# Kernel optimization log

Measured on AMD Instinct MI355X. Metric: run time of the kernel, lower is better.

Reference implementation:

```python
import jax, jax.numpy as jnp
import numpy as np

B, F, DOF, N_CLS = 256, 1024, 64, 1000

def setup_inputs() -> dict:
    key = jax.random.key(0)
    k1, k2 = jax.random.split(key)
    x = jax.random.normal(k1, (B, F), dtype=jnp.float32)
    # min/max of the input domain, as the dataloader scan would estimate on randn data
    min_x = jnp.array([-3.0], dtype=jnp.float32)
    max_x = jnp.array([3.0], dtype=jnp.float32)
    W = jax.random.normal(k2, (N_CLS, F * DOF), dtype=jnp.float32) * 0.01
    return {"x": x, "min_x": min_x, "max_x": max_x, "W": W, "dof": DOF}


def _lagrange_embed(x, min_x, max_x, dof):
    # 1D P1 Lagrange basis. simplices[t] = (t+1, t), t = 0..dof-2.
    b_, f_ = x.shape
    T = dof - 1
    h = 1.0 / T  # uniform mesh spacing on [0, 1]
    # normalize to unit interval, flatten to scalar stream of length b = B*F
    xn = ((x.reshape(-1, 1) - min_x) / (max_x - min_x)).reshape(-1)  # (b,)
    t = jnp.arange(T, dtype=xn.dtype)                                 # (T,)
    s = xn[:, None] / h                                               # (b, T) broadcastable
    lam0 = s - t            # barycentric coord of vertex t+1  (b, T)
    lam1 = (t + 1.0) - s    # barycentric coord of vertex t    (b, T)
    n2t = ((lam0 >= 0.0) & (lam1 >= 0.0)).astype(xn.dtype)            # (b, T)
    z = jnp.zeros((xn.shape[0], 1), dtype=xn.dtype)
    # mask[b, p] = number of active simplices touching vertex p (scatter of n2t to p=t and p=t+1)
    mask = jnp.concatenate([n2t, z], axis=1) + jnp.concatenate([z, n2t], axis=1)  # (b, dof)
    # shape_values[b, p] = sum over active simplices of the barycentric value at vertex p
    w0 = n2t * lam0  # goes to vertex p = t+1
    w1 = n2t * lam1  # goes to vertex p = t
    shape_vals = jnp.concatenate([w1, z], axis=1) + jnp.concatenate([z, w0], axis=1)  # (b, dof)
    basis = shape_vals / jnp.maximum(mask, 1.0)
    # rescale back to the input domain (n_features == 1, so (1,) broadcasts)
    emb = basis * (max_x - min_x) + min_x  # (b, dof)
    return emb.reshape(b_, f_ * dof)


def reference(x, min_x, max_x, W, dof):
    emb = jax.lax.stop_gradient(_lagrange_embed(x, min_x, max_x, dof))  # .detach() in torch
    return emb @ W.T  # bias-free Linear: (B, n_cls)
```

## Files before the change

### kernel.cpp

```cpp
#include <hip/hip_runtime.h>
#include <hip/hip_bf16.h>
#include <cstdint>

#define NB 256
#define NF 1024
#define NDOF 64
#define NCLS 1000
#define CTILE 128
#define FGROUP 32
#define NFB (NF / FGROUP)
#define ROWSTR 68

typedef __attribute__((ext_vector_type(8))) short short8;
typedef __attribute__((ext_vector_type(16))) float floatx16;

static __device__ inline unsigned short bfu(float f) {
    __hip_bfloat16 h = __float2bfloat16(f);
    union { __hip_bfloat16 h; unsigned short u; } cv;
    cv.h = h;
    return cv.u;
}

__global__ __launch_bounds__(256) void lagr_meta(
    const float* __restrict__ x, const float* __restrict__ mnp,
    const float* __restrict__ mxp, uint2* __restrict__ meta)
{
    __shared__ uint2 tile[32][33];
    int f0 = blockIdx.x * 32;
    int b0 = blockIdx.y * 32;
    int tid = threadIdx.x;
    float mn = mnp[0], mx = mxp[0];
    float scale = mx - mn;
    float inv = 63.0f / scale;

    int fl = tid & 31, br = tid >> 5;
#pragma unroll
    for (int i = 0; i < 4; ++i) {
        int bl = br + i * 8;
        float xv = x[(size_t)(b0 + bl) * NF + f0 + fl];
        float s = (xv - mn) * inv;
        float wA = 0.0f, wB = 0.0f;
        uint32_t t = 0u;
        if (s >= 0.0f && s <= 63.0f) {
            float tf = floorf(s);
            if (tf > 62.0f) tf = 62.0f;
            t  = (uint32_t)tf;
            wA = scale * (tf + 1.0f - s);
            wB = scale * (s - tf);
        }
        uint32_t P0 = (uint32_t)bfu(wA) | ((uint32_t)bfu(wB) << 16);
        tile[fl][bl] = make_uint2(P0, t);
    }
    __syncthreads();
    int bl = tid & 31, fr = tid >> 5;
#pragma unroll
    for (int i = 0; i < 4; ++i) {
        int f = fr + i * 8;
        meta[(size_t)(f0 + f) * NB + b0 + bl] = tile[f][bl];
    }
}

__global__ __launch_bounds__(512, 2) void lagr_main(
    const uint2* __restrict__ meta, const float* __restrict__ W,
    const float* __restrict__ mnp, float* __restrict__ part)
{
    __shared__ unsigned short wt[2][CTILE * ROWSTR];
    __shared__ float bias_s[CTILE];

    int tid  = threadIdx.x;
    int lane = tid & 63;
    int wave = tid >> 6;
    int half8 = (lane >> 5) << 3;
    int c0 = blockIdx.y * CTILE;
    int f0 = blockIdx.x * FGROUP;

    int cst = tid >> 2;
    int q4  = tid & 3;
    int crow = c0 + cst;
    if (crow > NCLS - 1) crow = NCLS - 1;
    const float* wrow = W + (size_t)crow * (NF * NDOF);

    floatx16 acc0, acc1, acc2, acc3;
#pragma unroll
    for (int r = 0; r < 16; ++r) { acc0[r] = 0.0f; acc1[r] = 0.0f; acc2[r] = 0.0f; acc3[r] = 0.0f; }
    float rowsum = 0.0f;

    float4 st[4];
    auto issue = [&](int f) {
        const float4* src = (const float4*)(wrow + ((size_t)f << 6)) + (q4 << 2);
        st[0] = src[0];
        st[1] = src[1];
        st[2] = src[2];
        st[3] = src[3];
    };
    auto commit = [&](unsigned short* buf) {
        float v[16] = { st[0].x, st[0].y, st[0].z, st[0].w,
                        st[1].x, st[1].y, st[1].z, st[1].w,
                        st[2].x, st[2].y, st[2].z, st[2].w,
                        st[3].x, st[3].y, st[3].z, st[3].w };
        uint32_t d[8];
#pragma unroll
        for (int i = 0; i < 8; ++i) {
            rowsum += v[2 * i] + v[2 * i + 1];
            d[i] = (uint32_t)bfu(v[2 * i]) | ((uint32_t)bfu(v[2 * i + 1]) << 16);
        }
        unsigned short* dst = buf + cst * ROWSTR + (q4 << 4);
        ((uint2*)dst)[0] = make_uint2(d[0], d[1]);
        ((uint2*)dst)[1] = make_uint2(d[2], d[3]);
        ((uint2*)dst)[2] = make_uint2(d[4], d[5]);
        ((uint2*)dst)[3] = make_uint2(d[6], d[7]);
    };

    unsigned short* cur = &wt[0][0];
    unsigned short* nxt = &wt[1][0];

    const uint2* mbase = meta + wave * 32 + (lane & 31);
    uint2 mcur = mbase[(size_t)f0 * NB];

    issue(f0);
    commit(cur);
    __syncthreads();

#pragma unroll 1
    for (int ch = 0; ch < FGROUP; ++ch) {
        int f = f0 + ch;
        bool more = (ch + 1 < FGROUP);
        if (more) issue(f + 1);
        uint2 mnext = mcur;
        if (more) mnext = mbase[(size_t)(f + 1) * NB];

        uint32_t P0 = mcur.x;
        uint32_t t  = mcur.y;
        uint32_t odd = t & 1u;
        uint32_t X0 = odd ? (P0 << 16) : P0;
        uint32_t X1 = odd ? (P0 >> 16) : 0u;
        int d0 = (int)(t & ~1u) - half8;

        short8 afrag[4];
#pragma unroll
        for (int kc = 0; kc < 4; ++kc) {
            union { uint32_t u[4]; short8 v; } a;
#pragma unroll
            for (int q = 0; q < 4; ++q) {
                int C = kc * 16 + 2 * q;
                a.u[q] = (d0 == C) ? X0 : (d0 == C - 2) ? X1 : 0u;
            }
            afrag[kc] = a.v;
        }

        const unsigned short* rb = cur + (lane & 31) * ROWSTR + half8;
#define CTBODY(CT, ACC) { \
        const unsigned short* r = rb + (CT) * 32 * ROWSTR; \
        _Pragma("unroll") \
        for (int kc = 0; kc < 4; ++kc) { \
            union { uint2 u2[2]; short8 v; } bf; \
            bf.u2[0] = *(const uint2*)(r + kc * 16); \
            bf.u2[1] = *(const uint2*)(r + kc * 16 + 4); \
            ACC = __builtin_amdgcn_mfma_f32_32x32x16_bf16(afrag[kc], bf.v, ACC, 0, 0, 0); \
        } }
        CTBODY(0, acc0)
        CTBODY(1, acc1)
        CTBODY(2, acc2)
        CTBODY(3, acc3)
#undef CTBODY

        if (more) commit(nxt);
        unsigned short* tmp = cur; cur = nxt; nxt = tmp;
        mcur = mnext;
        __syncthreads();
    }

    rowsum += __shfl_xor(rowsum, 1);
    rowsum += __shfl_xor(rowsum, 2);
    if (q4 == 0) bias_s[cst] = mnp[0] * rowsum;
    __syncthreads();

    float* pslice = part + (size_t)blockIdx.x * NB * NCLS;
    int col = lane & 31;
    int rowhi = (lane >> 5) << 2;
#define EPI(CT, ACC) { \
        int c = c0 + (CT) * 32 + col; \
        if (c < NCLS) { \
            float bias = bias_s[(CT) * 32 + col]; \
            _Pragma("unroll") \
            for (int r = 0; r < 16; ++r) { \
                int brow = (r & 3) + 8 * (r >> 2) + rowhi; \
                pslice[(size_t)(wave * 32 + brow) * NCLS + c] = ACC[r] + bias; \
            } } }
    EPI(0, acc0)
    EPI(1, acc1)
    EPI(2, acc2)
    EPI(3, acc3)
#undef EPI
}

__global__ __launch_bounds__(256) void lagr_reduce(
    const float* __restrict__ part, float* __restrict__ out)
{
    int i = blockIdx.x * blockDim.x + threadIdx.x;
    const float4* p = (const float4*)part;
    float4 a0 = make_float4(0.f, 0.f, 0.f, 0.f), a1 = a0, a2 = a0, a3 = a0;
    const int S = NB * NCLS / 4;
#pragma unroll
    for (int fb = 0; fb < NFB; fb += 4) {
        float4 v0 = p[(size_t)(fb + 0) * S + i];
        float4 v1 = p[(size_t)(fb + 1) * S + i];
        float4 v2 = p[(size_t)(fb + 2) * S + i];
        float4 v3 = p[(size_t)(fb + 3) * S + i];
        a0.x += v0.x; a0.y += v0.y; a0.z += v0.z; a0.w += v0.w;
        a1.x += v1.x; a1.y += v1.y; a1.z += v1.z; a1.w += v1.w;
        a2.x += v2.x; a2.y += v2.y; a2.z += v2.z; a2.w += v2.w;
        a3.x += v3.x; a3.y += v3.y; a3.z += v3.z; a3.w += v3.w;
    }
    float4 r;
    r.x = (a0.x + a1.x) + (a2.x + a3.x);
    r.y = (a0.y + a1.y) + (a2.y + a3.y);
    r.z = (a0.z + a1.z) + (a2.z + a3.z);
    r.w = (a0.w + a1.w) + (a2.w + a3.w);
    ((float4*)out)[i] = r;
}

extern "C" void kernel_launch(void* const* d_in, const int* in_sizes, int n_in,
                              void* d_out, int out_size, void* d_ws, size_t ws_size,
                              hipStream_t stream) {
    const float* x  = (const float*)d_in[0];
    const float* mn = (const float*)d_in[1];
    const float* mx = (const float*)d_in[2];
    const float* W  = (const float*)d_in[3];
    float* out = (float*)d_out;
    uint2* meta = (uint2*)d_ws;
    float* part = (float*)((char*)d_ws + (size_t)NF * NB * 8);

    lagr_meta<<<dim3(NF / 32, NB / 32), dim3(256), 0, stream>>>(x, mn, mx, meta);

    dim3 grid(NF / FGROUP, (NCLS + CTILE - 1) / CTILE);
    lagr_main<<<grid, dim3(512), 0, stream>>>(meta, W, mn, part);

    lagr_reduce<<<dim3(NB * NCLS / 4 / 256), dim3(256), 0, stream>>>(part, out);
}
```

Before: 385.2 us.

## Fuse embedding metadata computation into main GEMM kernel and XOR-swizzle weight LDS tile

Removes the separate meta kernel: each main block now computes the per-(b,f) bf16 weight pair and simplex index for its 32 features directly from x and stores them in shared memory. This drops one launch and the global round-trip of the meta buffer. The cost is that each of the 8 class-tile blocks per feature group repeats the x reads and arithmetic. The W tile in LDS also switches from a padded stride-68 layout to an XOR-swizzled 64-wide layout, so B fragments load as 16-byte reads and bank conflicts are avoided. Shared memory use grows, which may affect the two-blocks-per-CU occupancy.

```diff
diff --git a/kernel.cpp b/kernel.cpp
--- a/kernel.cpp
+++ b/kernel.cpp
@@ -9,7 +9,6 @@
 #define CTILE 128
 #define FGROUP 32
 #define NFB (NF / FGROUP)
-#define ROWSTR 68
 
 typedef __attribute__((ext_vector_type(8))) short short8;
 typedef __attribute__((ext_vector_type(16))) float floatx16;
@@ -21,61 +20,32 @@
     return cv.u;
 }
 
-__global__ __launch_bounds__(256) void lagr_meta(
+__global__ __launch_bounds__(512, 2) void lagr_main(
     const float* __restrict__ x, const float* __restrict__ mnp,
-    const float* __restrict__ mxp, uint2* __restrict__ meta)
+    const float* __restrict__ mxp, const float* __restrict__ W,
+    float* __restrict__ part)
 {
-    __shared__ uint2 tile[32][33];
-    int f0 = blockIdx.x * 32;
-    int b0 = blockIdx.y * 32;
-    int tid = threadIdx.x;
+    __shared__ unsigned short wt[2][128 * 64];
+    __shared__ uint32_t mP0[FGROUP][NB + 1];
+    __shared__ uint8_t  mT [FGROUP][NB + 8];
+    __shared__ float bias_s[CTILE];
+
+    int tid  = threadIdx.x;
+    int lane = tid & 63;
+    int wave = tid >> 6;
+    int hf   = lane >> 5;
+    int half8 = hf << 3;
+    int l7   = lane & 7;
+    int c0 = blockIdx.y * CTILE;
+    int f0 = blockIdx.x * FGROUP;
+
     float mn = mnp[0], mx = mxp[0];
     float scale = mx - mn;
     float inv = 63.0f / scale;
 
-    int fl = tid & 31, br = tid >> 5;
-#pragma unroll
-    for (int i = 0; i < 4; ++i) {
-        int bl = br + i * 8;
-        float xv = x[(size_t)(b0 + bl) * NF + f0 + fl];
-        float s = (xv - mn) * inv;
-        float wA = 0.0f, wB = 0.0f;
-        uint32_t t = 0u;
-        if (s >= 0.0f && s <= 63.0f) {
-            float tf = floorf(s);
-            if (tf > 62.0f) tf = 62.0f;
-            t  = (uint32_t)tf;
-            wA = scale * (tf + 1.0f - s);
-            wB = scale * (s - tf);
-        }
-        uint32_t P0 = (uint32_t)bfu(wA) | ((uint32_t)bfu(wB) << 16);
-        tile[fl][bl] = make_uint2(P0, t);
-    }
-    __syncthreads();
-    int bl = tid & 31, fr = tid >> 5;
-#pragma unroll
-    for (int i = 0; i < 4; ++i) {
-        int f = fr + i * 8;
-        meta[(size_t)(f0 + f) * NB + b0 + bl] = tile[f][bl];
-    }
-}
-
-__global__ __launch_bounds__(512, 2) void lagr_main(
-    const uint2* __restrict__ meta, const float* __restrict__ W,
-    const float* __restrict__ mnp, float* __restrict__ part)
-{
-    __shared__ unsigned short wt[2][CTILE * ROWSTR];
-    __shared__ float bias_s[CTILE];
-
-    int tid  = threadIdx.x;
-    int lane = tid & 63;
-    int wave = tid >> 6;
-    int half8 = (lane >> 5) << 3;
-    int c0 = blockIdx.y * CTILE;
-    int f0 = blockIdx.x * FGROUP;
-
     int cst = tid >> 2;
     int q4  = tid & 3;
+    int r7w = cst & 7;
     int crow = c0 + cst;
     if (crow > NCLS - 1) crow = NCLS - 1;
     const float* wrow = W + (size_t)crow * (NF * NDOF);
@@ -104,33 +74,50 @@
             rowsum += v[2 * i] + v[2 * i + 1];
             d[i] = (uint32_t)bfu(v[2 * i]) | ((uint32_t)bfu(v[2 * i + 1]) << 16);
         }
-        unsigned short* dst = buf + cst * ROWSTR + (q4 << 4);
-        ((uint2*)dst)[0] = make_uint2(d[0], d[1]);
-        ((uint2*)dst)[1] = make_uint2(d[2], d[3]);
-        ((uint2*)dst)[2] = make_uint2(d[4], d[5]);
-        ((uint2*)dst)[3] = make_uint2(d[6], d[7]);
+        unsigned short* row = buf + cst * 64;
+        *(uint4*)(row + (((2 * q4)     ^ r7w) << 3)) = make_uint4(d[0], d[1], d[2], d[3]);
+        *(uint4*)(row + (((2 * q4 + 1) ^ r7w) << 3)) = make_uint4(d[4], d[5], d[6], d[7]);
     };
 
     unsigned short* cur = &wt[0][0];
     unsigned short* nxt = &wt[1][0];
 
-    const uint2* mbase = meta + wave * 32 + (lane & 31);
-    uint2 mcur = mbase[(size_t)f0 * NB];
-
     issue(f0);
+
+    {
+        int fl = tid & 31, bq = tid >> 5;
+#pragma unroll
+        for (int i = 0; i < 16; ++i) {
+            int b = bq + i * 16;
+            float xv = x[(size_t)b * NF + f0 + fl];
+            float s = (xv - mn) * inv;
+            float wA = 0.0f, wB = 0.0f;
+            uint32_t t = 0u;
+            if (s >= 0.0f && s <= 63.0f) {
+                float tf = floorf(s);
+                if (tf > 62.0f) tf = 62.0f;
+                t  = (uint32_t)tf;
+                wA = scale * (tf + 1.0f - s);
+                wB = scale * (s - tf);
+            }
+            mP0[fl][b] = (uint32_t)bfu(wA) | ((uint32_t)bfu(wB) << 16);
+            mT[fl][b]  = (uint8_t)t;
+        }
+    }
+
     commit(cur);
     __syncthreads();
+
+    int mb = wave * 32 + (lane & 31);
 
 #pragma unroll 1
     for (int ch = 0; ch < FGROUP; ++ch) {
         int f = f0 + ch;
         bool more = (ch + 1 < FGROUP);
         if (more) issue(f + 1);
-        uint2 mnext = mcur;
-        if (more) mnext = mbase[(size_t)(f + 1) * NB];
-
-        uint32_t P0 = mcur.x;
-        uint32_t t  = mcur.y;
+
+        uint32_t P0 = mP0[ch][mb];
+        uint32_t t  = mT[ch][mb];
         uint32_t odd = t & 1u;
         uint32_t X0 = odd ? (P0 << 16) : P0;
         uint32_t X1 = odd ? (P0 >> 16) : 0u;
@@ -148,15 +135,12 @@
             afrag[kc] = a.v;
         }
 
-        const unsigned short* rb = cur + (lane & 31) * ROWSTR + half8;
 #define CTBODY(CT, ACC) { \
-        const unsigned short* r = rb + (CT) * 32 * ROWSTR; \
+        const unsigned short* rrow = cur + (size_t)((lane & 31) + 32 * (CT)) * 64; \
         _Pragma("unroll") \
         for (int kc = 0; kc < 4; ++kc) { \
-            union { uint2 u2[2]; short8 v; } bf; \
-            bf.u2[0] = *(const uint2*)(r + kc * 16); \
-            bf.u2[1] = *(const uint2*)(r + kc * 16 + 4); \
-            ACC = __builtin_amdgcn_mfma_f32_32x32x16_bf16(afrag[kc], bf.v, ACC, 0, 0, 0); \
+            short8 bv = *(const short8*)(rrow + (((2 * kc + hf) ^ l7) << 3)); \
+            ACC = __builtin_amdgcn_mfma_f32_32x32x16_bf16(afrag[kc], bv, ACC, 0, 0, 0); \
         } }
         CTBODY(0, acc0)
         CTBODY(1, acc1)
@@ -166,18 +150,17 @@
 
         if (more) commit(nxt);
         unsigned short* tmp = cur; cur = nxt; nxt = tmp;
-        mcur = mnext;
         __syncthreads();
     }
 
     rowsum += __shfl_xor(rowsum, 1);
     rowsum += __shfl_xor(rowsum, 2);
-    if (q4 == 0) bias_s[cst] = mnp[0] * rowsum;
+    if (q4 == 0) bias_s[cst] = mn * rowsum;
     __syncthreads();
 
     float* pslice = part + (size_t)blockIdx.x * NB * NCLS;
     int col = lane & 31;
-    int rowhi = (lane >> 5) << 2;
+    int rowhi = hf << 2;
 #define EPI(CT, ACC) { \
         int c = c0 + (CT) * 32 + col; \
         if (c < NCLS) { \
@@ -228,13 +211,10 @@
     const float* mx = (const float*)d_in[2];
     const float* W  = (const float*)d_in[3];
     float* out = (float*)d_out;
-    uint2* meta = (uint2*)d_ws;
-    float* part = (float*)((char*)d_ws + (size_t)NF * NB * 8);
-
-    lagr_meta<<<dim3(NF / 32, NB / 32), dim3(256), 0, stream>>>(x, mn, mx, meta);
+    float* part = (float*)d_ws;
 
     dim3 grid(NF / FGROUP, (NCLS + CTILE - 1) / CTILE);
-    lagr_main<<<grid, dim3(512), 0, stream>>>(meta, W, mn, part);
+    lagr_main<<<grid, dim3(512), 0, stream>>>(x, mn, mx, W, part);
 
     lagr_reduce<<<dim3(NB * NCLS / 4 / 256), dim3(256), 0, stream>>>(part, out);
 }
```

Result: slower. 396.8 us (+3.0%).

## Process two features per stage with XOR-swizzled LDS and 128-bit reads

Applied to the files above, without the earlier changes.

The main loop now stages two features of W per iteration, which halves the number of barriers and doubles the bytes each thread loads per prefetch. The LDS tile layout changes from padded rows (stride 68) to dense 64-element rows with an XOR swizzle on 8-element groups. This allows single 128-bit LDS writes and short8 reads for the MFMA B operand without bank conflicts. The cost is more registers for staging (8 float4s plus two A-fragment sets) and double the shared memory, which may lower occupancy below the 2-blocks target.

```diff
diff --git a/kernel.cpp b/kernel.cpp
--- a/kernel.cpp
+++ b/kernel.cpp
@@ -9,7 +9,7 @@
 #define CTILE 128
 #define FGROUP 32
 #define NFB (NF / FGROUP)
-#define ROWSTR 68
+#define SUBSZ (128 * 64)
 
 typedef __attribute__((ext_vector_type(8))) short short8;
 typedef __attribute__((ext_vector_type(16))) float floatx16;
@@ -64,18 +64,23 @@
     const uint2* __restrict__ meta, const float* __restrict__ W,
     const float* __restrict__ mnp, float* __restrict__ part)
 {
-    __shared__ unsigned short wt[2][CTILE * ROWSTR];
+    __shared__ unsigned short wt[2][2][SUBSZ];
     __shared__ float bias_s[CTILE];
 
     int tid  = threadIdx.x;
     int lane = tid & 63;
     int wave = tid >> 6;
-    int half8 = (lane >> 5) << 3;
+    int hf   = lane >> 5;
+    int half8 = hf << 3;
+    int l7   = lane & 7;
     int c0 = blockIdx.y * CTILE;
     int f0 = blockIdx.x * FGROUP;
 
     int cst = tid >> 2;
     int q4  = tid & 3;
+    int r7w = cst & 7;
+    int sub = q4 >> 1;
+    int gb  = (q4 & 1) << 2;
     int crow = c0 + cst;
     if (crow > NCLS - 1) crow = NCLS - 1;
     const float* wrow = W + (size_t)crow * (NF * NDOF);
@@ -85,88 +90,96 @@
     for (int r = 0; r < 16; ++r) { acc0[r] = 0.0f; acc1[r] = 0.0f; acc2[r] = 0.0f; acc3[r] = 0.0f; }
     float rowsum = 0.0f;
 
-    float4 st[4];
-    auto issue = [&](int f) {
-        const float4* src = (const float4*)(wrow + ((size_t)f << 6)) + (q4 << 2);
-        st[0] = src[0];
-        st[1] = src[1];
-        st[2] = src[2];
-        st[3] = src[3];
+    float4 st[8];
+    auto issue2 = [&](int f) {
+        const float4* src = (const float4*)(wrow + ((size_t)f << 6)) + (q4 << 3);
+#pragma unroll
+        for (int i = 0; i < 8; ++i) st[i] = src[i];
     };
-    auto commit = [&](unsigned short* buf) {
-        float v[16] = { st[0].x, st[0].y, st[0].z, st[0].w,
-                        st[1].x, st[1].y, st[1].z, st[1].w,
-                        st[2].x, st[2].y, st[2].z, st[2].w,
-                        st[3].x, st[3].y, st[3].z, st[3].w };
-        uint32_t d[8];
+    auto commit2 = [&](unsigned short* buf) {
+        float v[32];
 #pragma unroll
         for (int i = 0; i < 8; ++i) {
+            v[4 * i + 0] = st[i].x; v[4 * i + 1] = st[i].y;
+            v[4 * i + 2] = st[i].z; v[4 * i + 3] = st[i].w;
+        }
+        uint32_t d[16];
+#pragma unroll
+        for (int i = 0; i < 16; ++i) {
             rowsum += v[2 * i] + v[2 * i + 1];
             d[i] = (uint32_t)bfu(v[2 * i]) | ((uint32_t)bfu(v[2 * i + 1]) << 16);
         }
-        unsigned short* dst = buf + cst * ROWSTR + (q4 << 4);
-        ((uint2*)dst)[0] = make_uint2(d[0], d[1]);
-        ((uint2*)dst)[1] = make_uint2(d[2], d[3]);
-        ((uint2*)dst)[2] = make_uint2(d[4], d[5]);
-        ((uint2*)dst)[3] = make_uint2(d[6], d[7]);
+        unsigned short* row = buf + sub * SUBSZ + cst * 64;
+#pragma unroll
+        for (int g = 0; g < 4; ++g)
+            *(uint4*)(row + (((gb + g) ^ r7w) << 3)) =
+                make_uint4(d[4 * g], d[4 * g + 1], d[4 * g + 2], d[4 * g + 3]);
     };
 
-    unsigned short* cur = &wt[0][0];
-    unsigned short* nxt = &wt[1][0];
+    unsigned short* cur = &wt[0][0][0];
+    unsigned short* nxt = &wt[1][0][0];
 
     const uint2* mbase = meta + wave * 32 + (lane & 31);
-    uint2 mcur = mbase[(size_t)f0 * NB];
-
-    issue(f0);
-    commit(cur);
+    uint2 m0 = mbase[(size_t)(f0 + 0) * NB];
+    uint2 m1 = mbase[(size_t)(f0 + 1) * NB];
+
+    issue2(f0);
+    commit2(cur);
     __syncthreads();
 
 #pragma unroll 1
-    for (int ch = 0; ch < FGROUP; ++ch) {
-        int f = f0 + ch;
-        bool more = (ch + 1 < FGROUP);
-        if (more) issue(f + 1);
-        uint2 mnext = mcur;
-        if (more) mnext = mbase[(size_t)(f + 1) * NB];
-
-        uint32_t P0 = mcur.x;
-        uint32_t t  = mcur.y;
-        uint32_t odd = t & 1u;
-        uint32_t X0 = odd ? (P0 << 16) : P0;
-        uint32_t X1 = odd ? (P0 >> 16) : 0u;
-        int d0 = (int)(t & ~1u) - half8;
-
-        short8 afrag[4];
-#pragma unroll
-        for (int kc = 0; kc < 4; ++kc) {
-            union { uint32_t u[4]; short8 v; } a;
-#pragma unroll
-            for (int q = 0; q < 4; ++q) {
-                int C = kc * 16 + 2 * q;
-                a.u[q] = (d0 == C) ? X0 : (d0 == C - 2) ? X1 : 0u;
-            }
-            afrag[kc] = a.v;
-        }
-
-        const unsigned short* rb = cur + (lane & 31) * ROWSTR + half8;
-#define CTBODY(CT, ACC) { \
-        const unsigned short* r = rb + (CT) * 32 * ROWSTR; \
+    for (int g = 0; g < FGROUP / 2; ++g) {
+        int f = f0 + 2 * g;
+        bool more = (g + 1 < FGROUP / 2);
+        if (more) issue2(f + 2);
+        uint2 n0 = m0, n1 = m1;
+        if (more) {
+            n0 = mbase[(size_t)(f + 2) * NB];
+            n1 = mbase[(size_t)(f + 3) * NB];
+        }
+
+#define ABUILD(M, AF) { \
+        uint32_t P0 = (M).x; \
+        uint32_t t  = (M).y; \
+        uint32_t odd = t & 1u; \
+        uint32_t X0 = odd ? (P0 << 16) : P0; \
+        uint32_t X1 = odd ? (P0 >> 16) : 0u; \
+        int d0 = (int)(t & ~1u) - half8; \
         _Pragma("unroll") \
         for (int kc = 0; kc < 4; ++kc) { \
-            union { uint2 u2[2]; short8 v; } bf; \
-            bf.u2[0] = *(const uint2*)(r + kc * 16); \
-            bf.u2[1] = *(const uint2*)(r + kc * 16 + 4); \
-            ACC = __builtin_amdgcn_mfma_f32_32x32x16_bf16(afrag[kc], bf.v, ACC, 0, 0, 0); \
+            union { uint32_t u[4]; short8 v; } a; \
+            _Pragma("unroll") \
+            for (int q = 0; q < 4; ++q) { \
+                int C = kc * 16 + 2 * q; \
+                a.u[q] = (d0 == C) ? X0 : (d0 == C - 2) ? X1 : 0u; \
+            } \
+            AF[kc] = a.v; \
         } }
-        CTBODY(0, acc0)
-        CTBODY(1, acc1)
-        CTBODY(2, acc2)
-        CTBODY(3, acc3)
+        short8 af0[4], af1[4];
+        ABUILD(m0, af0)
+        ABUILD(m1, af1)
+#undef ABUILD
+
+#define CTBODY(SUB, AF, CT, ACC) { \
+        const unsigned short* rrow = cur + (SUB) * SUBSZ + (size_t)((lane & 31) + 32 * (CT)) * 64; \
+        _Pragma("unroll") \
+        for (int kc = 0; kc < 4; ++kc) { \
+            short8 bv = *(const short8*)(rrow + (((2 * kc + hf) ^ l7) << 3)); \
+            ACC = __builtin_amdgcn_mfma_f32_32x32x16_bf16(AF[kc], bv, ACC, 0, 0, 0); \
+        } }
+        CTBODY(0, af0, 0, acc0)
+        CTBODY(0, af0, 1, acc1)
+        CTBODY(0, af0, 2, acc2)
+        CTBODY(0, af0, 3, acc3)
+        CTBODY(1, af1, 0, acc0)
+        CTBODY(1, af1, 1, acc1)
+        CTBODY(1, af1, 2, acc2)
+        CTBODY(1, af1, 3, acc3)
 #undef CTBODY
 
-        if (more) commit(nxt);
+        if (more) commit2(nxt);
         unsigned short* tmp = cur; cur = nxt; nxt = tmp;
-        mcur = mnext;
+        m0 = n0; m1 = n1;
         __syncthreads();
     }
 
@@ -177,7 +190,7 @@
 
     float* pslice = part + (size_t)blockIdx.x * NB * NCLS;
     int col = lane & 31;
-    int rowhi = (lane >> 5) << 2;
+    int rowhi = hf << 2;
 #define EPI(CT, ACC) { \
         int c = c0 + (CT) * 32 + col; \
         if (c < NCLS) { \
```

Result: no change. 381.2 us (-1.1%).
